# Optimization experiments

Hardware: AMD Instinct MI355X
Metric: run time of the kernel (lower is better)

## Reference

```python
import jax, jax.numpy as jnp
import numpy as np

SCALE = 0.05  # temperature from the module
C, NUM, IN_DIM, HID = 64, 128, 768, 128


def _l2norm(x):
    n = jnp.sqrt(jnp.sum(x * x, axis=-1, keepdims=True))
    return x / jnp.maximum(n, 1e-12)


def setup_inputs() -> dict:
    key = jax.random.key(0)
    k1, k2, k3, k4 = jax.random.split(key, 4)
    embeds = jax.random.normal(k1, (C, NUM, IN_DIM), dtype=jnp.float32)
    head_w = jax.random.normal(k2, (HID, IN_DIM), dtype=jnp.float32) * (1.0 / np.sqrt(IN_DIM))
    head_b = jax.random.normal(k3, (HID,), dtype=jnp.float32) * 0.01
    proto = jax.random.normal(k4, (C, HID), dtype=jnp.float32) * (1.0 / np.sqrt(HID))
    return {"embeds": embeds, "head_w": head_w, "head_b": head_b, "proto": proto}


def reference(embeds, head_w, head_b, proto):
    # x = head(embeds): [C, num, hid]
    x = jnp.einsum('cni,hi->cnh', embeds, head_w) + head_b
    num = x.shape[1]
    num_classes = proto.shape[0]

    nx = _l2norm(x)            # [C, num, d]
    nproto = _l2norm(proto)    # [C, d]

    # ---- prototype contrastive term (loop over i in num, fused) ----
    # sim_mat[c, n, k] = exp(cos(x[c,n], proto[k]) / scale)
    sim_mat = jnp.exp(jnp.einsum('cnd,kd->cnk', nx, nproto) / SCALE)
    pos = jnp.diagonal(sim_mat, axis1=0, axis2=2)      # [num, C], pos[n,c] = sim_mat[c,n,c]
    total = sim_mat.sum(-1).T                           # [num, C]
    loss = -jnp.log(pos / total).sum()
    loss = loss / (num * num_classes * num_classes)

    # ---- instance-instance term (loop over i in num_classes, fused) ----
    # S[a, m, b, n] = exp(cos(x[a,m], x[b,n]) / scale)
    S = jnp.exp(jnp.einsum('amd,bnd->ambn', nx, nx) / SCALE)
    # per-anchor-class i: pos_ins[m, n] = S[i, m, i, n]
    pos_ins = jnp.diagonal(S, axis1=0, axis2=2)         # [m, n, C(i)]
    sumA = jnp.transpose(S.sum(0), (0, 2, 1))           # [m, n, C(i)]
    neg_ins = (sumA - pos_ins).sum(0)                   # [n, C(i)]
    loss_ins = -jnp.log(pos_ins / (pos_ins + neg_ins[None, :, :])).sum()
    loss_ins = loss_ins / (num * num_classes * num * num_classes)

    return loss + loss_ins
```

## Files before the change

### kernel.cpp

```cpp
#include <hip/hip_runtime.h>
#include <math.h>

#define SCALE_INV 20.0f
#define EXPK 28.853900817779268f
#define LN2F 0.6931471805599453f

typedef __bf16 bf16x8 __attribute__((ext_vector_type(8)));
typedef float  f32x4  __attribute__((ext_vector_type(4)));

__global__ __launch_bounds__(256) void k_headnorm(const float* __restrict__ e,
                                                  const float* __restrict__ w,
                                                  const float* __restrict__ hb,
                                                  __bf16* __restrict__ nxb,
                                                  __bf16* __restrict__ nxe,
                                                  float* __restrict__ cspart,
                                                  float* __restrict__ accs) {
  __shared__ __bf16 Ab[32 * 72];
  __shared__ __bf16 Bb[128 * 72];
  __shared__ float  xt[32 * 132];
  __shared__ float  hbl[128];
  const int t  = threadIdx.x;
  const int rt = blockIdx.x;
  if (t < 128) hbl[t] = hb[t];
  if (t < 32) cspart[rt * 32 + t] = 0.0f;
  if (rt == 0 && t >= 128 && t < 132) accs[t - 128] = 0.0f;

  const int arow = t >> 3, akoff = (t & 7) * 8;
  const int brow = t >> 1, bkoff = (t & 1) * 32;
  float4 ar[2], br[8];
  {
    const float* p = &e[(rt * 32 + arow) * 768 + akoff];
    ar[0] = *(const float4*)p; ar[1] = *(const float4*)(p + 4);
    const float* q = &w[brow * 768 + bkoff];
    for (int i = 0; i < 8; i++) br[i] = *(const float4*)(q + 4 * i);
  }

  const int wv = t >> 6, lane = t & 63;
  const int quad = lane >> 4, lrow = lane & 15;
  const int rb = wv & 1, cb = wv >> 1;
  f32x4 acc[4];
  f32x4 zero = {0.f, 0.f, 0.f, 0.f};
  for (int j = 0; j < 4; j++) acc[j] = zero;

  for (int it = 0; it < 12; it++) {
    {
      __bf16 ta[8];
      const float* f = (const float*)ar;
      for (int i = 0; i < 8; i++) ta[i] = (__bf16)f[i];
      *(bf16x8*)&Ab[arow * 72 + akoff] = *(bf16x8*)ta;
      const float* g = (const float*)br;
      for (int seg = 0; seg < 4; seg++) {
        __bf16 tb[8];
        for (int i = 0; i < 8; i++) tb[i] = (__bf16)g[seg * 8 + i];
        *(bf16x8*)&Bb[brow * 72 + bkoff + seg * 8] = *(bf16x8*)tb;
      }
    }
    __syncthreads();
    if (it < 11) {
      int kb = (it + 1) * 64;
      const float* p = &e[(rt * 32 + arow) * 768 + kb + akoff];
      ar[0] = *(const float4*)p; ar[1] = *(const float4*)(p + 4);
      const float* q = &w[brow * 768 + kb + bkoff];
      for (int i = 0; i < 8; i++) br[i] = *(const float4*)(q + 4 * i);
    }
    for (int kc = 0; kc < 2; kc++) {
      bf16x8 a = *(const bf16x8*)&Ab[(rb * 16 + lrow) * 72 + kc * 32 + quad * 8];
      for (int j = 0; j < 4; j++) {
        bf16x8 b = *(const bf16x8*)&Bb[(cb * 64 + j * 16 + lrow) * 72 + kc * 32 + quad * 8];
        acc[j] = __builtin_amdgcn_mfma_f32_16x16x32_bf16(a, b, acc[j], 0, 0, 0);
      }
    }
    __syncthreads();
  }

  for (int j = 0; j < 4; j++)
    for (int r = 0; r < 4; r++) {
      int row = rb * 16 + quad * 4 + r;
      int col = cb * 64 + j * 16 + lrow;
      xt[row * 132 + col] = acc[j][r] + hbl[col];
    }
  __syncthreads();
  {
    int row = t >> 3, c0 = (t & 7) * 16;
    float v[16];
    float s = 0.0f;
    for (int i = 0; i < 4; i++) {
      float4 f = *(const float4*)&xt[row * 132 + c0 + i * 4];
      v[i * 4] = f.x; v[i * 4 + 1] = f.y; v[i * 4 + 2] = f.z; v[i * 4 + 3] = f.w;
    }
    for (int i = 0; i < 16; i++) s += v[i] * v[i];
    s += __shfl_xor(s, 1, 64);
    s += __shfl_xor(s, 2, 64);
    s += __shfl_xor(s, 4, 64);
    float inv = 1.0f / fmaxf(sqrtf(s), 1e-12f);
    __bf16 o[16], oe[16];
    for (int i = 0; i < 16; i++) {
      float nv = v[i] * inv;
      o[i]  = (__bf16)nv;
      oe[i] = (__bf16)(nv * EXPK);
    }
    __bf16* dst = &nxb[(rt * 32 + row) * 128 + c0];
    *(bf16x8*)dst       = *(bf16x8*)o;
    *(bf16x8*)(dst + 8) = *(bf16x8*)(o + 8);
    __bf16* dse = &nxe[(rt * 32 + row) * 128 + c0];
    *(bf16x8*)dse       = *(bf16x8*)oe;
    *(bf16x8*)(dse + 8) = *(bf16x8*)(oe + 8);
  }
}

__global__ __launch_bounds__(256) void k_colsum(const __bf16* __restrict__ nxb,
                                                const __bf16* __restrict__ nxe,
                                                const float* __restrict__ proto,
                                                float* __restrict__ cspart,
                                                float* __restrict__ posD,
                                                float* __restrict__ accs) {
  __shared__ __bf16 At[128 * 136];
  __shared__ __bf16 Bt[128 * 136];
  __shared__ float  colpart[4 * 128];
  const int t    = threadIdx.x;
  const int cj   = blockIdx.x;
  const int rs   = blockIdx.y;
  const int w    = t >> 6, lane = t & 63;
  const int quad = lane >> 4, lrow = lane & 15;
  const int sr   = t >> 4, sseg = t & 15;

  if (rs < 8) {
    for (int it = 0; it < 8; it++) {
      int r = sr + it * 16;
      *(bf16x8*)&Bt[r * 136 + sseg * 8] =
          *(const bf16x8*)&nxe[(cj * 128 + r) * 128 + sseg * 8];
    }
    int tiles[4], nt = 0;
    for (int mm = 0; mm < 4; mm++) {
      int m = rs * 4 + 1 + mm;
      if (m < 32 || cj < 32) tiles[nt++] = (cj + m) & 63;
    }
    bf16x8 pre[8];
    for (int it = 0; it < 8; it++)
      pre[it] = *(const bf16x8*)&nxb[(tiles[0] * 128 + sr + it * 16) * 128 + sseg * 8];

    float colacc[8];
    for (int j = 0; j < 8; j++) colacc[j] = 0.0f;

    for (int ti = 0; ti < nt; ti++) {
      const int ci = tiles[ti];
      for (int it = 0; it < 8; it++)
        *(bf16x8*)&At[(sr + it * 16) * 136 + sseg * 8] = pre[it];
      __syncthreads();
      if (ti + 1 < nt) {
        int cn = tiles[ti + 1];
        for (int it = 0; it < 8; it++)
          pre[it] = *(const bf16x8*)&nxb[(cn * 128 + sr + it * 16) * 128 + sseg * 8];
      }
      f32x4 acc[2][8];
      f32x4 zero = {0.0f, 0.0f, 0.0f, 0.0f};
      for (int i = 0; i < 2; i++)
        for (int j = 0; j < 8; j++) acc[i][j] = zero;
      for (int kc = 0; kc < 4; kc++) {
        bf16x8 a0 = *(const bf16x8*)&At[(w * 32 + lrow) * 136 + kc * 32 + quad * 8];
        bf16x8 a1 = *(const bf16x8*)&At[(w * 32 + 16 + lrow) * 136 + kc * 32 + quad * 8];
        for (int j = 0; j < 8; j++) {
          bf16x8 b = *(const bf16x8*)&Bt[(j * 16 + lrow) * 136 + kc * 32 + quad * 8];
          acc[0][j] = __builtin_amdgcn_mfma_f32_16x16x32_bf16(a0, b, acc[0][j], 0, 0, 0);
          acc[1][j] = __builtin_amdgcn_mfma_f32_16x16x32_bf16(a1, b, acc[1][j], 0, 0, 0);
        }
      }
      float rsum[2][4];
      for (int i = 0; i < 2; i++)
        for (int r = 0; r < 4; r++) rsum[i][r] = 0.0f;
      for (int i = 0; i < 2; i++)
        for (int j = 0; j < 8; j++)
          for (int r = 0; r < 4; r++) {
            float ev = exp2f(acc[i][j][r]);
            colacc[j]  += ev;
            rsum[i][r] += ev;
          }
      for (int i = 0; i < 2; i++)
        for (int r = 0; r < 4; r++) {
          float v = rsum[i][r];
          v += __shfl_xor(v, 1, 64);
          v += __shfl_xor(v, 2, 64);
          v += __shfl_xor(v, 4, 64);
          v += __shfl_xor(v, 8, 64);
          if (lrow == 0)
            atomicAdd(&cspart[ci * 128 + w * 32 + i * 16 + quad * 4 + r], v);
        }
      __syncthreads();
    }

    for (int j = 0; j < 8; j++) {
      float v = colacc[j];
      v += __shfl_xor(v, 16, 64);
      v += __shfl_xor(v, 32, 64);
      if (lane < 16) colpart[w * 128 + j * 16 + lane] = v;
    }
    __syncthreads();
    if (t < 128) {
      float s = colpart[t] + colpart[128 + t] + colpart[256 + t] + colpart[384 + t];
      atomicAdd(&cspart[cj * 128 + t], s);
    }
  } else if (rs == 8) {
    for (int it = 0; it < 8; it++) {
      int r = sr + it * 16;
      *(bf16x8*)&At[r * 136 + sseg * 8] =
          *(const bf16x8*)&nxb[(cj * 128 + r) * 128 + sseg * 8];
      *(bf16x8*)&Bt[r * 136 + sseg * 8] =
          *(const bf16x8*)&nxe[(cj * 128 + r) * 128 + sseg * 8];
    }
    __syncthreads();
    f32x4 acc[2][8];
    f32x4 zero = {0.0f, 0.0f, 0.0f, 0.0f};
    for (int i = 0; i < 2; i++)
      for (int j = 0; j < 8; j++) acc[i][j] = zero;
    for (int kc = 0; kc < 4; kc++) {
      bf16x8 a0 = *(const bf16x8*)&At[(w * 32 + lrow) * 136 + kc * 32 + quad * 8];
      bf16x8 a1 = *(const bf16x8*)&At[(w * 32 + 16 + lrow) * 136 + kc * 32 + quad * 8];
      for (int j = 0; j < 8; j++) {
        bf16x8 b = *(const bf16x8*)&Bt[(j * 16 + lrow) * 136 + kc * 32 + quad * 8];
        acc[0][j] = __builtin_amdgcn_mfma_f32_16x16x32_bf16(a0, b, acc[0][j], 0, 0, 0);
        acc[1][j] = __builtin_amdgcn_mfma_f32_16x16x32_bf16(a1, b, acc[1][j], 0, 0, 0);
      }
    }
    for (int i = 0; i < 2; i++)
      for (int j = 0; j < 8; j++)
        for (int r = 0; r < 4; r++) {
          int row = w * 32 + i * 16 + quad * 4 + r;
          int col = j * 16 + lrow;
          posD[cj * 16384 + row * 128 + col] = acc[i][j][r];
        }
  } else {
    for (int it = 0; it < 8; it++) {
      int r = sr + it * 16;
      *(bf16x8*)&At[r * 136 + sseg * 8] =
          *(const bf16x8*)&nxb[(cj * 128 + r) * 128 + sseg * 8];
    }
    {
      const int rw = t >> 2, part = t & 3;
      float v[32];
      float s = 0.0f;
      const float* p = &proto[rw * 128 + part * 32];
      for (int i = 0; i < 8; i++) {
        float4 f = *(const float4*)(p + 4 * i);
        v[i * 4] = f.x; v[i * 4 + 1] = f.y; v[i * 4 + 2] = f.z; v[i * 4 + 3] = f.w;
        s += f.x * f.x + f.y * f.y + f.z * f.z + f.w * f.w;
      }
      s += __shfl_xor(s, 1, 64);
      s += __shfl_xor(s, 2, 64);
      float inv = EXPK / fmaxf(sqrtf(s), 1e-12f);
      __bf16 o[32];
      for (int i = 0; i < 32; i++) o[i] = (__bf16)(v[i] * inv);
      __bf16* dst = &Bt[rw * 136 + part * 32];
      for (int i = 0; i < 4; i++) *(bf16x8*)(dst + i * 8) = *(bf16x8*)(o + i * 8);
    }
    __syncthreads();
    f32x4 acc_p[2][4];
    f32x4 zero = {0.0f, 0.0f, 0.0f, 0.0f};
    for (int i = 0; i < 2; i++)
      for (int j = 0; j < 4; j++) acc_p[i][j] = zero;
    for (int kc = 0; kc < 4; kc++) {
      bf16x8 a0 = *(const bf16x8*)&At[(w * 32 + lrow) * 136 + kc * 32 + quad * 8];
      bf16x8 a1 = *(const bf16x8*)&At[(w * 32 + 16 + lrow) * 136 + kc * 32 + quad * 8];
      for (int j = 0; j < 4; j++) {
        bf16x8 b = *(const bf16x8*)&Bt[(j * 16 + lrow) * 136 + kc * 32 + quad * 8];
        acc_p[0][j] = __builtin_amdgcn_mfma_f32_16x16x32_bf16(a0, b, acc_p[0][j], 0, 0, 0);
        acc_p[1][j] = __builtin_amdgcn_mfma_f32_16x16x32_bf16(a1, b, acc_p[1][j], 0, 0, 0);
      }
    }
    float wacc0 = 0.0f;
    for (int i = 0; i < 2; i++) {
      for (int r = 0; r < 4; r++) {
        float tot = 0.0f;
        for (int j = 0; j < 4; j++) tot += exp2f(acc_p[i][j][r]);
        tot += __shfl_xor(tot, 1, 64);
        tot += __shfl_xor(tot, 2, 64);
        tot += __shfl_xor(tot, 4, 64);
        tot += __shfl_xor(tot, 8, 64);
        if (lrow == 0) wacc0 += logf(tot);
      }
      const int jc = cj >> 4, colc = cj & 15;
      if (lrow == colc) {
        float sd = 0.0f;
        switch (jc) {
          case 0: for (int r = 0; r < 4; r++) sd += acc_p[i][0][r]; break;
          case 1: for (int r = 0; r < 4; r++) sd += acc_p[i][1][r]; break;
          case 2: for (int r = 0; r < 4; r++) sd += acc_p[i][2][r]; break;
          default: for (int r = 0; r < 4; r++) sd += acc_p[i][3][r]; break;
        }
        wacc0 -= sd * LN2F;
      }
    }
    for (int off = 32; off; off >>= 1) wacc0 += __shfl_xor(wacc0, off, 64);
    if (lane == 0) atomicAdd(&accs[0], wacc0);
  }
}

__global__ __launch_bounds__(256) void k_last(const float* __restrict__ posD,
                                              const float* __restrict__ cspart,
                                              float* __restrict__ accs,
                                              float* __restrict__ out) {
  __shared__ float negl[128];
  __shared__ float wred[4];
  const int b = blockIdx.x, t = threadIdx.x;
  const int cls = b >> 2, m0 = (b & 3) * 32;
  if (t < 128) negl[t] = cspart[cls * 128 + t];
  __syncthreads();
  const float* base = &posD[cls * 16384 + m0 * 128];
  float wacc = 0.0f;
  for (int it = 0; it < 4; it++) {
    int idx = (it * 256 + t) * 4;
    float4 d = *(const float4*)&base[idx];
    int n = idx & 127;
    wacc += log1pf(negl[n]     * exp2f(-d.x));
    wacc += log1pf(negl[n + 1] * exp2f(-d.y));
    wacc += log1pf(negl[n + 2] * exp2f(-d.z));
    wacc += log1pf(negl[n + 3] * exp2f(-d.w));
  }
  for (int off = 32; off; off >>= 1) wacc += __shfl_xor(wacc, off, 64);
  if ((t & 63) == 0) wred[t >> 6] = wacc;
  __syncthreads();
  if (t == 0) {
    atomicAdd(&accs[1], wred[0] + wred[1] + wred[2] + wred[3]);
    __threadfence();
    unsigned int old = atomicAdd((unsigned int*)&accs[3], 1u);
    if (old == 255u) {
      __threadfence();
      float a0 = atomicAdd(&accs[0], 0.0f);
      float a1 = atomicAdd(&accs[1], 0.0f);
      out[0] = a0 * (1.0f / 524288.0f) + a1 * (1.0f / 67108864.0f);
    }
  }
}

extern "C" void kernel_launch(void* const* d_in, const int* in_sizes, int n_in,
                              void* d_out, int out_size, void* d_ws, size_t ws_size,
                              hipStream_t stream) {
  const float* e  = (const float*)d_in[0];
  const float* w  = (const float*)d_in[1];
  const float* hb = (const float*)d_in[2];
  const float* pr = (const float*)d_in[3];
  char* ws = (char*)d_ws;
  __bf16* nxb    = (__bf16*)ws;
  __bf16* nxe    = (__bf16*)(ws + (2 << 20));
  float*  cspart = (float*)(ws + (4 << 20));
  float*  accs   = (float*)(ws + (4 << 20) + (64 << 10));
  float*  posD   = (float*)(ws + (5 << 20));
  float*  out    = (float*)d_out;

  k_headnorm<<<256, 256, 0, stream>>>(e, w, hb, nxb, nxe, cspart, accs);
  k_colsum<<<dim3(64, 10), 256, 0, stream>>>(nxb, nxe, pr, cspart, posD, accs);
  k_last<<<256, 256, 0, stream>>>(posD, cspart, accs, out);
}
```

Measured before the change: 131.4 us.

## Pre-convert head weights to bf16 in a prep kernel and double the K tile

Adds a small prep kernel that converts head_w to bf16 once per call and zeroes the accumulators, so each of the 256 head blocks loads half the weight bytes and skips the per-block fp32-to-bf16 conversion. The GEMM K tile grows from 64 to 128, halving the number of loop iterations and barriers. The cost is an extra kernel launch and a workspace round-trip for the converted weights, plus larger shared-memory tiles that may lower occupancy.

Result: faster. 124.2 us (median of 2 runs) (-5.5%).

```diff
diff --git a/kernel.cpp b/kernel.cpp
--- a/kernel.cpp
+++ b/kernel.cpp
@@ -6,33 +6,44 @@
 #define LN2F 0.6931471805599453f
 
 typedef __bf16 bf16x8 __attribute__((ext_vector_type(8)));
+typedef __bf16 bf16x4 __attribute__((ext_vector_type(4)));
 typedef float  f32x4  __attribute__((ext_vector_type(4)));
 
+__global__ __launch_bounds__(256) void k_prep(const float* __restrict__ w,
+                                              __bf16* __restrict__ wb,
+                                              float* __restrict__ cspart,
+                                              float* __restrict__ accs) {
+  const int b = blockIdx.x, t = threadIdx.x;
+  int i = (b * 256 + t) * 4;
+  float4 f = *(const float4*)&w[i];
+  __bf16 o[4] = {(__bf16)f.x, (__bf16)f.y, (__bf16)f.z, (__bf16)f.w};
+  *(bf16x4*)&wb[i] = *(bf16x4*)o;
+  if (b < 64 && t < 128) cspart[b * 128 + t] = 0.0f;
+  if (b == 95 && t < 4) accs[t] = 0.0f;
+}
+
 __global__ __launch_bounds__(256) void k_headnorm(const float* __restrict__ e,
-                                                  const float* __restrict__ w,
+                                                  const __bf16* __restrict__ wb,
                                                   const float* __restrict__ hb,
                                                   __bf16* __restrict__ nxb,
-                                                  __bf16* __restrict__ nxe,
-                                                  float* __restrict__ cspart,
-                                                  float* __restrict__ accs) {
-  __shared__ __bf16 Ab[32 * 72];
-  __shared__ __bf16 Bb[128 * 72];
+                                                  __bf16* __restrict__ nxe) {
+  __shared__ __bf16 Ab[32 * 136];
+  __shared__ __bf16 Bb[128 * 136];
   __shared__ float  xt[32 * 132];
   __shared__ float  hbl[128];
   const int t  = threadIdx.x;
   const int rt = blockIdx.x;
   if (t < 128) hbl[t] = hb[t];
-  if (t < 32) cspart[rt * 32 + t] = 0.0f;
-  if (rt == 0 && t >= 128 && t < 132) accs[t - 128] = 0.0f;
-
-  const int arow = t >> 3, akoff = (t & 7) * 8;
-  const int brow = t >> 1, bkoff = (t & 1) * 32;
-  float4 ar[2], br[8];
+
+  const int arow = t >> 3, akoff = (t & 7) * 16;
+  const int brow = t >> 1, bkoff = (t & 1) * 64;
+  float4 ar[4];
+  bf16x8 brg[8];
   {
     const float* p = &e[(rt * 32 + arow) * 768 + akoff];
-    ar[0] = *(const float4*)p; ar[1] = *(const float4*)(p + 4);
-    const float* q = &w[brow * 768 + bkoff];
-    for (int i = 0; i < 8; i++) br[i] = *(const float4*)(q + 4 * i);
+    for (int i = 0; i < 4; i++) ar[i] = *(const float4*)(p + 4 * i);
+    const __bf16* q = &wb[brow * 768 + bkoff];
+    for (int i = 0; i < 8; i++) brg[i] = *(const bf16x8*)(q + 8 * i);
   }
 
   const int wv = t >> 6, lane = t & 63;
@@ -42,31 +53,28 @@
   f32x4 zero = {0.f, 0.f, 0.f, 0.f};
   for (int j = 0; j < 4; j++) acc[j] = zero;
 
-  for (int it = 0; it < 12; it++) {
+  for (int it = 0; it < 6; it++) {
     {
-      __bf16 ta[8];
+      __bf16 ta[16];
       const float* f = (const float*)ar;
-      for (int i = 0; i < 8; i++) ta[i] = (__bf16)f[i];
-      *(bf16x8*)&Ab[arow * 72 + akoff] = *(bf16x8*)ta;
-      const float* g = (const float*)br;
-      for (int seg = 0; seg < 4; seg++) {
-        __bf16 tb[8];
-        for (int i = 0; i < 8; i++) tb[i] = (__bf16)g[seg * 8 + i];
-        *(bf16x8*)&Bb[brow * 72 + bkoff + seg * 8] = *(bf16x8*)tb;
-      }
-    }
-    __syncthreads();
-    if (it < 11) {
-      int kb = (it + 1) * 64;
+      for (int i = 0; i < 16; i++) ta[i] = (__bf16)f[i];
+      *(bf16x8*)&Ab[arow * 136 + akoff]     = *(bf16x8*)ta;
+      *(bf16x8*)&Ab[arow * 136 + akoff + 8] = *(bf16x8*)(ta + 8);
+      for (int seg = 0; seg < 8; seg++)
+        *(bf16x8*)&Bb[brow * 136 + bkoff + seg * 8] = brg[seg];
+    }
+    __syncthreads();
+    if (it < 5) {
+      int kb = (it + 1) * 128;
       const float* p = &e[(rt * 32 + arow) * 768 + kb + akoff];
-      ar[0] = *(const float4*)p; ar[1] = *(const float4*)(p + 4);
-      const float* q = &w[brow * 768 + kb + bkoff];
-      for (int i = 0; i < 8; i++) br[i] = *(const float4*)(q + 4 * i);
-    }
-    for (int kc = 0; kc < 2; kc++) {
-      bf16x8 a = *(const bf16x8*)&Ab[(rb * 16 + lrow) * 72 + kc * 32 + quad * 8];
+      for (int i = 0; i < 4; i++) ar[i] = *(const float4*)(p + 4 * i);
+      const __bf16* q = &wb[brow * 768 + kb + bkoff];
+      for (int i = 0; i < 8; i++) brg[i] = *(const bf16x8*)(q + 8 * i);
+    }
+    for (int kc = 0; kc < 4; kc++) {
+      bf16x8 a = *(const bf16x8*)&Ab[(rb * 16 + lrow) * 136 + kc * 32 + quad * 8];
       for (int j = 0; j < 4; j++) {
-        bf16x8 b = *(const bf16x8*)&Bb[(cb * 64 + j * 16 + lrow) * 72 + kc * 32 + quad * 8];
+        bf16x8 b = *(const bf16x8*)&Bb[(cb * 64 + j * 16 + lrow) * 136 + kc * 32 + quad * 8];
         acc[j] = __builtin_amdgcn_mfma_f32_16x16x32_bf16(a, b, acc[j], 0, 0, 0);
       }
     }
@@ -344,9 +352,11 @@
   float*  cspart = (float*)(ws + (4 << 20));
   float*  accs   = (float*)(ws + (4 << 20) + (64 << 10));
   float*  posD   = (float*)(ws + (5 << 20));
+  __bf16* wb     = (__bf16*)(ws + (9 << 20));
   float*  out    = (float*)d_out;
 
-  k_headnorm<<<256, 256, 0, stream>>>(e, w, hb, nxb, nxe, cspart, accs);
+  k_prep<<<96, 256, 0, stream>>>(w, wb, cspart, accs);
+  k_headnorm<<<256, 256, 0, stream>>>(e, wb, hb, nxb, nxe);
   k_colsum<<<dim3(64, 10), 256, 0, stream>>>(nxb, nxe, pr, cspart, posD, accs);
   k_last<<<256, 256, 0, stream>>>(posD, cspart, accs, out);
 }
```
